# Performance work log

Hardware: AMD Instinct MI355X
Metric: run time of the kernel (lower is better)

## Reference

```python
import jax, jax.numpy as jnp
import numpy as np
from jax import lax

NUM_CLASSES = 2
IOU_THRESH = 0.5
SCORE_THRESH = 0.5
K_CAND = 512        # per-class candidate pool fed to greedy NMS
MAX_PER_CLASS = 100
MAX_TOTAL = 100


def setup_inputs() -> dict:
    key = jax.random.key(0)
    k1, k2, k3 = jax.random.split(key, 3)
    B = 64
    pred_s1 = jax.random.normal(k1, (B, 19, 19, 3, 5 + NUM_CLASSES), dtype=jnp.float32)
    pred_s2 = jax.random.normal(k2, (B, 38, 38, 3, 5 + NUM_CLASSES), dtype=jnp.float32)
    pred_s3 = jax.random.normal(k3, (B, 76, 76, 3, 5 + NUM_CLASSES), dtype=jnp.float32)
    # standard YOLOv3 anchors (pixels) normalized by input size 608
    anchors_px = np.array([[10, 13], [16, 30], [33, 23], [30, 61], [62, 45],
                           [59, 119], [116, 90], [156, 198], [373, 326]], np.float32)
    anchors = jnp.asarray(anchors_px / 608.0)
    return {"pred_s1": pred_s1, "pred_s2": pred_s2, "pred_s3": pred_s3, "anchors": anchors}


def _decode(pred, anch):
    # pred: [B, g, g, A, 5+C]; anch: [A, 2] normalized wh
    g = pred.shape[1]
    box_xy = jax.nn.sigmoid(pred[..., 0:2])
    box_wh = jnp.exp(pred[..., 2:4]) * anch          # broadcast [A,2]
    obj = jax.nn.sigmoid(pred[..., 4:5])
    cls = jax.nn.sigmoid(pred[..., 5:])
    gx, gy = jnp.meshgrid(jnp.arange(g), jnp.arange(g))   # 'xy' indexing, as tf.meshgrid
    grid = jnp.stack([gx, gy], axis=-1)[:, :, None, :].astype(pred.dtype)  # [g,g,1,2]
    xy = (box_xy + grid) / jnp.float32(g)
    x1y1 = xy - box_wh / 2.0
    x2y2 = x1y1 + box_wh                              # YoloNMS: wh + xy(top-left)
    boxes = jnp.concatenate([x1y1, x2y2], axis=-1)    # [B,g,g,A,4]
    scores = obj * cls                                # [B,g,g,A,C]
    B = pred.shape[0]
    return boxes.reshape(B, -1, 4), scores.reshape(B, -1, NUM_CLASSES)


def _pairwise_iou(b):
    # b: [K,4] in (x1,y1,x2,y2); returns [K,K]
    a = b[:, None, :]
    c = b[None, :, :]
    iw = jnp.clip(jnp.minimum(a[..., 2], c[..., 2]) - jnp.maximum(a[..., 0], c[..., 0]), 0.0)
    ih = jnp.clip(jnp.minimum(a[..., 3], c[..., 3]) - jnp.maximum(a[..., 1], c[..., 1]), 0.0)
    inter = iw * ih
    area = jnp.clip(b[:, 2] - b[:, 0], 0.0) * jnp.clip(b[:, 3] - b[:, 1], 0.0)
    union = area[:, None] + area[None, :] - inter
    return inter / jnp.maximum(union, 1e-9)


def _nms_one_class(boxes, scores):
    # boxes: [N,4], scores: [N] -> candidate boxes/scores/keep mask, each len K_CAND
    sc, idx = lax.top_k(scores, K_CAND)               # sorted descending
    bx = boxes[idx]
    iou = lax.stop_gradient(_pairwise_iou(bx))
    valid = sc > SCORE_THRESH
    def body(i, keep):
        suppressed = jnp.any(keep & (iou[i] > IOU_THRESH))
        return keep.at[i].set(valid[i] & ~suppressed)
    keep = lax.fori_loop(0, K_CAND, body, jnp.zeros((K_CAND,), jnp.bool_))
    keep = keep & (jnp.cumsum(keep) <= MAX_PER_CLASS)
    return bx, sc, keep


def _nms_one_image(boxes, scores):
    # boxes: [N,4], scores: [N,C]
    bk, sk, keep = jax.vmap(_nms_one_class, in_axes=(None, 1))(boxes, scores)  # [C,K,*]
    sm = jnp.where(keep, sk, -1.0)
    cls_ids = jnp.broadcast_to(jnp.arange(NUM_CLASSES)[:, None], (NUM_CLASSES, K_CAND))
    sf = sm.reshape(-1)
    bf = bk.reshape(-1, 4)
    cf = cls_ids.reshape(-1)
    ts, ti = lax.top_k(sf, MAX_TOTAL)
    kept = ts > 0.0
    out_boxes = jnp.where(kept[:, None], jnp.clip(bf[ti], 0.0, 1.0), 0.0)  # clip_boxes=True
    out_scores = jnp.where(kept, ts, 0.0)
    out_classes = jnp.where(kept, cf[ti].astype(jnp.float32), 0.0)
    return out_boxes, out_scores, out_classes, jnp.sum(kept).astype(jnp.int32)


def reference(pred_s1, pred_s2, pred_s3, anchors):
    # scale masks: grid19 -> anchors[6:9], grid38 -> anchors[3:6], grid76 -> anchors[0:3]
    b1, s1 = _decode(pred_s1, anchors[6:9])
    b2, s2 = _decode(pred_s2, anchors[3:6])
    b3, s3 = _decode(pred_s3, anchors[0:3])
    boxes = jnp.concatenate([b1, b2, b3], axis=1)     # [B,N,4]
    scores = jnp.concatenate([s1, s2, s3], axis=1)    # [B,N,C]
    return jax.vmap(_nms_one_image)(boxes, scores)
```

## Files before the change

### kernel.cpp

```cpp
#include <hip/hip_runtime.h>
#include <cstdint>
#include <cstddef>

#define NTOT   22743
#define N1     1083
#define N12    5415
#define BATCH  64
#define KCAND  512
#define NSEG   16
#define SEGLEN 1422
#define CAPS   384
#define CAP    4096
#define MAXPC  100
#define MAXTOT 100
#define KITER  6

__device__ __forceinline__ float sigmoidf(float x) { return 1.0f / (1.0f + expf(-x)); }
__device__ __forceinline__ int SK4(int j) { return j + ((j >> 6) << 2); }

__global__ __launch_bounds__(256) void score_filter_kernel(
    const float* __restrict__ p1, const float* __restrict__ p2,
    const float* __restrict__ p3, uint2* __restrict__ cand,
    uint32_t* __restrict__ counts)
{
  const int blk  = blockIdx.x;
  const int b    = blk >> 4;
  const int s    = blk & 15;
  const int tid  = threadIdx.x;
  const int lane = tid & 63;

  __shared__ uint2    lst[2][CAPS];
  __shared__ uint32_t lcnt[2];

  if (tid < 2) lcnt[tid] = 0u;
  __syncthreads();

  const int beg = s * SEGLEN;
  const int end = (beg + SEGLEN < NTOT) ? beg + SEGLEN : NTOT;

  float4 v[KITER];
  #pragma unroll
  for (int k = 0; k < KITER; ++k) {
    int i0 = beg + tid + k * 256;
    if (i0 < end) {
      const float* p; int local, per;
      if (i0 < N1)       { p = p1; local = i0;        per = 1083; }
      else if (i0 < N12) { p = p2; local = i0 - N1;   per = 4332; }
      else               { p = p3; local = i0 - N12;  per = 17328; }
      const float* q = p + ((size_t)b * per + local) * 7;
      v[k] = *(const float4*)(q + 3);
    } else {
      v[k] = make_float4(0.f, -1.f, 0.f, 0.f);
    }
  }

  #pragma unroll
  for (int k = 0; k < KITER; ++k) {
    int i0 = beg + tid + k * 256;
    float s0 = 0.f, s1 = 0.f;
    float q4 = v[k].y;
    if (q4 > 0.f) {
      float obj = sigmoidf(q4);
      s0 = obj * sigmoidf(v[k].z);
      s1 = obj * sigmoidf(v[k].w);
    }
    #pragma unroll
    for (int c = 0; c < 2; c++) {
      float sc = (c == 0) ? s0 : s1;
      bool pred = sc > 0.5f;
      unsigned long long m = __ballot(pred ? 1 : 0);
      if (m != 0ull) {
        int leader = (int)__ffsll(m) - 1;
        uint32_t base = 0u;
        if (lane == leader) base = atomicAdd(&lcnt[c], (uint32_t)__popcll(m));
        base = (uint32_t)__shfl((int)base, leader);
        if (pred) {
          uint32_t off = base + (uint32_t)__popcll(m & ((1ull << lane) - 1ull));
          if (off < CAPS) lst[c][off] = make_uint2(__float_as_uint(sc), (uint32_t)i0);
        }
      }
    }
  }
  __syncthreads();

  #pragma unroll
  for (int c = 0; c < 2; c++) {
    uint32_t cnt = lcnt[c]; if (cnt > CAPS) cnt = CAPS;
    uint2* dst = cand + ((size_t)((b * 2 + c) * NSEG + s)) * CAPS;
    for (uint32_t i = tid; i < cnt; i += 256) dst[i] = lst[c][i];
    if (tid == 0) counts[(b * 2 + c) * NSEG + s] = cnt;
  }
}

__device__ void decode_box(const float* __restrict__ p1, const float* __restrict__ p2,
                           const float* __restrict__ p3, const float* __restrict__ anch,
                           int b, int i, float bb[4])
{
  const float* p; int local, g, abase, per;
  if (i < N1)       { p = p1; local = i;       g = 19; abase = 6; per = 1083; }
  else if (i < N12) { p = p2; local = i - N1;  g = 38; abase = 3; per = 4332; }
  else              { p = p3; local = i - N12; g = 76; abase = 0; per = 17328; }
  const float* q = p + ((size_t)b * per + local) * 7;
  int a    = local % 3;
  int cell = local / 3;
  int col  = cell % g;
  int row  = cell / g;
  float aw = anch[(abase + a) * 2 + 0];
  float ah = anch[(abase + a) * 2 + 1];
  float x = (sigmoidf(q[0]) + (float)col) / (float)g;
  float y = (sigmoidf(q[1]) + (float)row) / (float)g;
  float w = expf(q[2]) * aw;
  float h = expf(q[3]) * ah;
  float x1 = x - w * 0.5f;
  float y1 = y - h * 0.5f;
  bb[0] = x1; bb[1] = y1; bb[2] = x1 + w; bb[3] = y1 + h;
}

__global__ __launch_bounds__(1024) void nms_kernel(
    const uint2* __restrict__ cand, const uint32_t* __restrict__ counts,
    const float* __restrict__ p1, const float* __restrict__ p2,
    const float* __restrict__ p3, const float* __restrict__ anch,
    float* __restrict__ selScore, float* __restrict__ selBox,
    int* __restrict__ selRank, int* __restrict__ selCount)
{
  const int bc   = blockIdx.x;
  const int b    = bc >> 1;
  const int tid  = threadIdx.x;
  const int lane = tid & 63;

  __shared__ __attribute__((aligned(16))) unsigned long long bord[CAP];
  __shared__ __attribute__((aligned(16))) float bx1[544];
  __shared__ __attribute__((aligned(16))) float by1[544];
  __shared__ __attribute__((aligned(16))) float bx2[544];
  __shared__ __attribute__((aligned(16))) float by2[544];
  __shared__ __attribute__((aligned(16))) float ar[544];
  __shared__ uint32_t           skey[512];
  __shared__ unsigned long long msk[128][9];
  __shared__ unsigned long long kword[8];
  __shared__ uint32_t           hist3[768];
  __shared__ uint32_t           svar[8];

  if (tid < 768) hist3[tid] = 0u;
  if (tid == 0) svar[5] = 0u;
  if (tid < 512) {
    skey[tid] = 0u; int p = SK4(tid);
    bx1[p] = 0.f; by1[p] = 0.f; bx2[p] = 0.f; by2[p] = 0.f; ar[p] = 0.f;
  }

  uint32_t pc[17];
  pc[0] = 0;
  #pragma unroll
  for (int t = 0; t < 16; ++t) {
    uint32_t c = counts[bc * NSEG + t];
    if (c > CAPS) c = CAPS;
    pc[t + 1] = pc[t] + c;
  }
  const int n = ((int)pc[16] < CAP) ? (int)pc[16] : CAP;
  const int limit = (n < KCAND) ? n : KCAND;

  unsigned long long v0, v1, v2, v3;
  auto loadc = [&](int i) -> unsigned long long {
    if (i >= n) return 0ull;
    uint32_t ps = 0; int s = 0;
    #pragma unroll
    for (int t = 1; t < 16; ++t) {
      bool ge = (uint32_t)i >= pc[t];
      s += (int)ge; ps = ge ? pc[t] : ps;
    }
    uint2 e = cand[(size_t)(bc * NSEG + s) * CAPS + (i - (int)ps)];
    return ((unsigned long long)e.x << 32) | (uint32_t)(~e.y);
  };
  v0 = loadc(tid); v1 = loadc(tid + 1024); v2 = loadc(tid + 2048); v3 = loadc(tid + 3072);
  __syncthreads();

  uint32_t* bcnt = hist3;
  uint32_t* boff = hist3 + 256;
  uint32_t* bpre = hist3 + 512;

  #define BKT(vv) ((uint32_t)(((vv) >> 47) & 255u))
  if (v0) atomicAdd(&bcnt[BKT(v0)], 1u);
  if (v1) atomicAdd(&bcnt[BKT(v1)], 1u);
  if (v2) atomicAdd(&bcnt[BKT(v2)], 1u);
  if (v3) atomicAdd(&bcnt[BKT(v3)], 1u);
  __syncthreads();

  if (tid < 64) {
    uint32_t h0 = bcnt[lane * 4 + 0], h1 = bcnt[lane * 4 + 1];
    uint32_t h2 = bcnt[lane * 4 + 2], h3 = bcnt[lane * 4 + 3];
    uint32_t s3 = h3, s2 = h2 + s3, s1 = h1 + s2, s0 = h0 + s1;
    uint32_t acc = s0;
    #pragma unroll
    for (int o = 1; o < 64; o <<= 1) {
      uint32_t vv = __shfl_down(acc, (unsigned)o);
      acc += (lane + o < 64) ? vv : 0u;
    }
    uint32_t above = acc - s0;
    bpre[lane * 4 + 0] = above + s1;
    bpre[lane * 4 + 1] = above + s2;
    bpre[lane * 4 + 2] = above + s3;
    bpre[lane * 4 + 3] = above;
  }
  __syncthreads();

  if (v0) bord[bpre[BKT(v0)] + atomicAdd(&boff[BKT(v0)], 1u)] = v0;
  if (v1) bord[bpre[BKT(v1)] + atomicAdd(&boff[BKT(v1)], 1u)] = v1;
  if (v2) bord[bpre[BKT(v2)] + atomicAdd(&boff[BKT(v2)], 1u)] = v2;
  if (v3) bord[bpre[BKT(v3)] + atomicAdd(&boff[BKT(v3)], 1u)] = v3;
  __syncthreads();

  auto rankdec = [&](unsigned long long e) {
    if (e == 0ull) return;
    const uint32_t B = BKT(e);
    const uint32_t lo = bpre[B], sz = bcnt[B];
    int rank = (int)lo;
    if ((int)lo < KCAND) {
      for (uint32_t j = lo; j < lo + sz; ++j) rank += (int)(bord[j] > e);
      if (rank < KCAND) {
        int idx = (int)(~(uint32_t)e);
        float bb[4];
        decode_box(p1, p2, p3, anch, b, idx, bb);
        int p = SK4(rank);
        bx1[p] = bb[0]; by1[p] = bb[1]; bx2[p] = bb[2]; by2[p] = bb[3];
        ar[p]  = fmaxf(bb[2] - bb[0], 0.f) * fmaxf(bb[3] - bb[1], 0.f);
        skey[rank] = (uint32_t)(e >> 32);
      }
    }
  };
  rankdec(v0); rankdec(v1); rankdec(v2); rankdec(v3);
  #undef BKT
  __syncthreads();

  unsigned long long Kw = 0ull;
  int kept = 0;
  const int r = tid & 127;
  const int w = tid >> 7;

  for (int ch = 0; ch < 4; ++ch) {
    const int base = ch * 128;
    int rows = limit - base; if (rows > 128) rows = 128;

    if (r < rows) {
      const int i = base + r;
      if (w <= (i >> 6)) {
        const int ip = SK4(i);
        const float x1i = bx1[ip], y1i = by1[ip], x2i = bx2[ip], y2i = by2[ip];
        const float ai = ar[ip];
        unsigned long long mrow = 0ull;
        #pragma unroll
        for (int m4 = 0; m4 < 16; ++m4) {
          const int j0 = (w << 6) + (m4 << 2);
          const int a  = j0 + (w << 2);
          float4 X1 = *(const float4*)&bx1[a];
          float4 Y1 = *(const float4*)&by1[a];
          float4 X2 = *(const float4*)&bx2[a];
          float4 Y2 = *(const float4*)&by2[a];
          float4 AR = *(const float4*)&ar[a];
          #define IOU_BIT(JX1,JY1,JX2,JY2,JAR,J)                              \
            { float iw = fminf(x2i,(JX2)) - fmaxf(x1i,(JX1));                 \
              float ih = fminf(y2i,(JY2)) - fmaxf(y1i,(JY1));                 \
              iw = fmaxf(iw,0.f); ih = fmaxf(ih,0.f);                        \
              float inter = iw*ih;                                            \
              float uni = fmaxf(ai + (JAR) - inter, 1e-9f);                   \
              if ((inter/uni > 0.5f) && ((J) < i))                            \
                mrow |= 1ull << ((J) & 63); }
          IOU_BIT(X1.x, Y1.x, X2.x, Y2.x, AR.x, j0 + 0)
          IOU_BIT(X1.y, Y1.y, X2.y, Y2.y, AR.y, j0 + 1)
          IOU_BIT(X1.z, Y1.z, X2.z, Y2.z, AR.z, j0 + 2)
          IOU_BIT(X1.w, Y1.w, X2.w, Y2.w, AR.w, j0 + 3)
          #undef IOU_BIT
        }
        msk[r][w] = mrow;
      } else {
        msk[r][w] = 0ull;
      }
    }
    __syncthreads();

    if (tid < 64) {
      bool stop = false;
      for (int g = 0; g < 16 && !stop; ++g) {
        int r0 = g * 8;
        if (r0 >= rows) break;
        unsigned long long wbuf[8];
        #pragma unroll
        for (int k2 = 0; k2 < 8; ++k2)
          wbuf[k2] = (lane < 8 && (r0 + k2) < rows) ? msk[r0 + k2][lane] : 0ull;
        #pragma unroll
        for (int k2 = 0; k2 < 8; ++k2) {
          if (!stop) {
            int rr = r0 + k2;
            if (rr >= rows) { stop = true; }
            else {
              int i = base + rr;
              bool ov = (Kw & wbuf[k2]) != 0ull;
              if (!__any(ov)) {
                if (lane == (i >> 6)) Kw |= 1ull << (i & 63);
                if (++kept >= MAXPC) stop = true;
              }
            }
          }
        }
      }
      if (lane == 0) svar[5] = (kept >= MAXPC || (base + (rows > 0 ? rows : 0)) >= limit) ? 1u : 0u;
    }
    __syncthreads();
    if (svar[5] != 0u) break;
  }

  if (tid < 8) kword[tid] = Kw;
  __syncthreads();

  if (tid < 512) {
    int rr = tid;
    int wr = rr >> 6;
    unsigned long long kw = kword[wr];
    if ((kw >> (rr & 63)) & 1ull) {
      uint32_t p = 0;
      for (int ww = 0; ww < wr; ++ww) p += (uint32_t)__popcll(kword[ww]);
      p += (uint32_t)__popcll(kw & ((1ull << (rr & 63)) - 1ull));
      selScore[bc * MAXPC + p] = __uint_as_float(skey[rr]);
      selRank[bc * MAXPC + p]  = rr;
      int rp = SK4(rr);
      float* o = &selBox[(size_t)(bc * MAXPC + p) * 4];
      o[0] = bx1[rp]; o[1] = by1[rp]; o[2] = bx2[rp]; o[3] = by2[rp];
    }
  }
  if (tid == 0) {
    uint32_t tot = 0;
    for (int ww = 0; ww < 8; ++ww) tot += (uint32_t)__popcll(kword[ww]);
    selCount[bc] = (int)tot;
  }
}

__global__ __launch_bounds__(256) void merge_kernel(
    const float* __restrict__ selScore, const float* __restrict__ selBox,
    const int* __restrict__ selRank, const int* __restrict__ selCount,
    float* __restrict__ out)
{
  const int b   = blockIdx.x;
  const int tid = threadIdx.x;
  __shared__ float    es[200];
  __shared__ uint32_t ek[200];
  __shared__ float    eb[200][4];
  const int c0  = selCount[b * 2 + 0];
  const int c1  = selCount[b * 2 + 1];
  const int tot = c0 + c1;

  if (tid < tot) {
    int cls  = (tid < c0) ? 0 : 1;
    int slot = (cls == 0) ? tid : (tid - c0);
    int src  = (b * 2 + cls) * MAXPC + slot;
    es[tid] = selScore[src];
    ek[tid] = (uint32_t)(cls * KCAND + selRank[src]);
    eb[tid][0] = selBox[(size_t)src * 4 + 0];
    eb[tid][1] = selBox[(size_t)src * 4 + 1];
    eb[tid][2] = selBox[(size_t)src * 4 + 2];
    eb[tid][3] = selBox[(size_t)src * 4 + 3];
  }
  __syncthreads();

  float* outBoxes  = out;
  float* outScores = out + (size_t)BATCH * MAXTOT * 4;
  float* outCls    = outScores + (size_t)BATCH * MAXTOT;
  float* outCnt    = outCls + (size_t)BATCH * MAXTOT;
  const int filled = (tot < MAXTOT) ? tot : MAXTOT;

  if (tid < tot) {
    float    s  = es[tid];
    uint32_t fk = ek[tid];
    int rank = 0;
    for (int j = 0; j < tot; j++)
      rank += (int)((es[j] > s) || (es[j] == s && ek[j] < fk));
    if (rank < MAXTOT) {
      outScores[b * MAXTOT + rank] = s;
      outCls[b * MAXTOT + rank]    = (float)(fk >> 9);
      float* ob = &outBoxes[(size_t)(b * MAXTOT + rank) * 4];
      ob[0] = fminf(fmaxf(eb[tid][0], 0.f), 1.f);
      ob[1] = fminf(fmaxf(eb[tid][1], 0.f), 1.f);
      ob[2] = fminf(fmaxf(eb[tid][2], 0.f), 1.f);
      ob[3] = fminf(fmaxf(eb[tid][3], 0.f), 1.f);
    }
  }
  if (tid >= filled && tid < MAXTOT) {
    outScores[b * MAXTOT + tid] = 0.f;
    outCls[b * MAXTOT + tid]    = 0.f;
    float* ob = &outBoxes[(size_t)(b * MAXTOT + tid) * 4];
    ob[0] = 0.f; ob[1] = 0.f; ob[2] = 0.f; ob[3] = 0.f;
  }
  if (tid == 0) outCnt[b] = (float)filled;
}

extern "C" void kernel_launch(void* const* d_in, const int* in_sizes, int n_in,
                              void* d_out, int out_size, void* d_ws, size_t ws_size,
                              hipStream_t stream)
{
  const float* p1   = (const float*)d_in[0];
  const float* p2   = (const float*)d_in[1];
  const float* p3   = (const float*)d_in[2];
  const float* anch = (const float*)d_in[3];

  uint8_t* ws = (uint8_t*)d_ws;
  uint32_t* counts = (uint32_t*)ws;
  uint2*    cand   = (uint2*)(ws + 16384);
  uint8_t*  wp     = ws + 16384 + (size_t)128 * NSEG * CAPS * 8;
  float*    selScore = (float*)wp;         wp += (size_t)BATCH * 2 * MAXPC * 4;
  float*    selBox   = (float*)wp;         wp += (size_t)BATCH * 2 * MAXPC * 16;
  int*      selRank  = (int*)wp;           wp += (size_t)BATCH * 2 * MAXPC * 4;
  int*      selCount = (int*)wp;

  score_filter_kernel<<<BATCH * NSEG, 256, 0, stream>>>(p1, p2, p3, cand, counts);
  nms_kernel<<<BATCH * 2, 1024, 0, stream>>>(cand, counts, p1, p2, p3, anch,
                                             selScore, selBox, selRank, selCount);
  merge_kernel<<<BATCH, 256, 0, stream>>>(selScore, selBox, selRank, selCount,
                                          (float*)d_out);
}
```

Before: 56.98 us.

## Fuse score filtering into per-class NMS kernel, dropping candidate workspace

Removes the separate score-filter kernel and its global candidate buffer. Each NMS block now streams its image's predictions directly, scores one class, and compacts passing candidates into shared memory with ballot-based appends, then reuses that buffer for the bucket sort. This saves a kernel launch and the global write/read round trip. In exchange, only 128 blocks scan the input (each image is read twice, once per class), so the filter phase has less parallelism. Block-to-(image,class) mapping is also permuted so the two class blocks of an image are spaced apart.

```diff
diff --git a/kernel.cpp b/kernel.cpp
--- a/kernel.cpp
+++ b/kernel.cpp
@@ -7,89 +7,26 @@
 #define N12    5415
 #define BATCH  64
 #define KCAND  512
-#define NSEG   16
-#define SEGLEN 1422
-#define CAPS   384
 #define CAP    4096
 #define MAXPC  100
 #define MAXTOT 100
-#define KITER  6
+#define KIT2   23
 
 __device__ __forceinline__ float sigmoidf(float x) { return 1.0f / (1.0f + expf(-x)); }
 __device__ __forceinline__ int SK4(int j) { return j + ((j >> 6) << 2); }
 
-__global__ __launch_bounds__(256) void score_filter_kernel(
-    const float* __restrict__ p1, const float* __restrict__ p2,
-    const float* __restrict__ p3, uint2* __restrict__ cand,
-    uint32_t* __restrict__ counts)
-{
-  const int blk  = blockIdx.x;
-  const int b    = blk >> 4;
-  const int s    = blk & 15;
-  const int tid  = threadIdx.x;
-  const int lane = tid & 63;
-
-  __shared__ uint2    lst[2][CAPS];
-  __shared__ uint32_t lcnt[2];
-
-  if (tid < 2) lcnt[tid] = 0u;
-  __syncthreads();
-
-  const int beg = s * SEGLEN;
-  const int end = (beg + SEGLEN < NTOT) ? beg + SEGLEN : NTOT;
-
-  float4 v[KITER];
-  #pragma unroll
-  for (int k = 0; k < KITER; ++k) {
-    int i0 = beg + tid + k * 256;
-    if (i0 < end) {
-      const float* p; int local, per;
-      if (i0 < N1)       { p = p1; local = i0;        per = 1083; }
-      else if (i0 < N12) { p = p2; local = i0 - N1;   per = 4332; }
-      else               { p = p3; local = i0 - N12;  per = 17328; }
-      const float* q = p + ((size_t)b * per + local) * 7;
-      v[k] = *(const float4*)(q + 3);
-    } else {
-      v[k] = make_float4(0.f, -1.f, 0.f, 0.f);
-    }
-  }
-
-  #pragma unroll
-  for (int k = 0; k < KITER; ++k) {
-    int i0 = beg + tid + k * 256;
-    float s0 = 0.f, s1 = 0.f;
-    float q4 = v[k].y;
-    if (q4 > 0.f) {
-      float obj = sigmoidf(q4);
-      s0 = obj * sigmoidf(v[k].z);
-      s1 = obj * sigmoidf(v[k].w);
-    }
-    #pragma unroll
-    for (int c = 0; c < 2; c++) {
-      float sc = (c == 0) ? s0 : s1;
-      bool pred = sc > 0.5f;
-      unsigned long long m = __ballot(pred ? 1 : 0);
-      if (m != 0ull) {
-        int leader = (int)__ffsll(m) - 1;
-        uint32_t base = 0u;
-        if (lane == leader) base = atomicAdd(&lcnt[c], (uint32_t)__popcll(m));
-        base = (uint32_t)__shfl((int)base, leader);
-        if (pred) {
-          uint32_t off = base + (uint32_t)__popcll(m & ((1ull << lane) - 1ull));
-          if (off < CAPS) lst[c][off] = make_uint2(__float_as_uint(sc), (uint32_t)i0);
-        }
-      }
-    }
-  }
-  __syncthreads();
-
-  #pragma unroll
-  for (int c = 0; c < 2; c++) {
-    uint32_t cnt = lcnt[c]; if (cnt > CAPS) cnt = CAPS;
-    uint2* dst = cand + ((size_t)((b * 2 + c) * NSEG + s)) * CAPS;
-    for (uint32_t i = tid; i < cnt; i += 256) dst[i] = lst[c][i];
-    if (tid == 0) counts[(b * 2 + c) * NSEG + s] = cnt;
-  }
+__device__ __forceinline__ float4 loadrow(const float* __restrict__ p1,
+                                          const float* __restrict__ p2,
+                                          const float* __restrict__ p3,
+                                          int b, int i)
+{
+  if (i >= NTOT) return make_float4(0.f, -1.f, 0.f, 0.f);
+  const float* p; int local, per;
+  if (i < N1)       { p = p1; local = i;        per = 1083; }
+  else if (i < N12) { p = p2; local = i - N1;   per = 4332; }
+  else              { p = p3; local = i - N12;  per = 17328; }
+  const float* q = p + ((size_t)b * per + local) * 7;
+  return *(const float4*)(q + 3);
 }
 
 __device__ void decode_box(const float* __restrict__ p1, const float* __restrict__ p2,
@@ -116,19 +53,20 @@
   bb[0] = x1; bb[1] = y1; bb[2] = x1 + w; bb[3] = y1 + h;
 }
 
-__global__ __launch_bounds__(1024) void nms_kernel(
-    const uint2* __restrict__ cand, const uint32_t* __restrict__ counts,
+__global__ __launch_bounds__(1024) void nms_fused_kernel(
     const float* __restrict__ p1, const float* __restrict__ p2,
     const float* __restrict__ p3, const float* __restrict__ anch,
     float* __restrict__ selScore, float* __restrict__ selBox,
     int* __restrict__ selRank, int* __restrict__ selCount)
 {
-  const int bc   = blockIdx.x;
-  const int b    = bc >> 1;
+  const int u    = blockIdx.x;
+  const int b    = (u & 7) | ((u >> 4) << 3);
+  const int c    = (u >> 3) & 1;
+  const int bc   = b * 2 + c;
   const int tid  = threadIdx.x;
   const int lane = tid & 63;
 
-  __shared__ __attribute__((aligned(16))) unsigned long long bord[CAP];
+  __shared__ __attribute__((aligned(16))) unsigned long long kvw[CAP];
   __shared__ __attribute__((aligned(16))) float bx1[544];
   __shared__ __attribute__((aligned(16))) float by1[544];
   __shared__ __attribute__((aligned(16))) float bx2[544];
@@ -141,36 +79,47 @@
   __shared__ uint32_t           svar[8];
 
   if (tid < 768) hist3[tid] = 0u;
-  if (tid == 0) svar[5] = 0u;
+  if (tid == 0) { svar[0] = 0u; svar[5] = 0u; }
   if (tid < 512) {
     skey[tid] = 0u; int p = SK4(tid);
     bx1[p] = 0.f; by1[p] = 0.f; bx2[p] = 0.f; by2[p] = 0.f; ar[p] = 0.f;
   }
-
-  uint32_t pc[17];
-  pc[0] = 0;
-  #pragma unroll
-  for (int t = 0; t < 16; ++t) {
-    uint32_t c = counts[bc * NSEG + t];
-    if (c > CAPS) c = CAPS;
-    pc[t + 1] = pc[t] + c;
-  }
-  const int n = ((int)pc[16] < CAP) ? (int)pc[16] : CAP;
+  __syncthreads();
+
+  float4 cur = loadrow(p1, p2, p3, b, tid);
+  for (int k = 0; k < KIT2; ++k) {
+    float4 nxt = (k + 1 < KIT2) ? loadrow(p1, p2, p3, b, (k + 1) * 1024 + tid)
+                                : make_float4(0.f, -1.f, 0.f, 0.f);
+    const int i0 = k * 1024 + tid;
+    float sc = 0.f;
+    float q4 = cur.y;
+    if (q4 > 0.f) {
+      float obj = sigmoidf(q4);
+      sc = obj * sigmoidf((c == 0) ? cur.z : cur.w);
+    }
+    bool pred = sc > 0.5f;
+    unsigned long long m = __ballot(pred ? 1 : 0);
+    if (m != 0ull) {
+      int leader = (int)__ffsll(m) - 1;
+      uint32_t base = 0u;
+      if (lane == leader) base = atomicAdd(&svar[0], (uint32_t)__popcll(m));
+      base = (uint32_t)__shfl((int)base, leader);
+      if (pred) {
+        uint32_t off = base + (uint32_t)__popcll(m & ((1ull << lane) - 1ull));
+        if (off < CAP)
+          kvw[off] = ((unsigned long long)__float_as_uint(sc) << 32) | (uint32_t)(~(uint32_t)i0);
+      }
+    }
+    cur = nxt;
+  }
+  __syncthreads();
+  const int n = ((int)svar[0] < CAP) ? (int)svar[0] : CAP;
   const int limit = (n < KCAND) ? n : KCAND;
 
-  unsigned long long v0, v1, v2, v3;
-  auto loadc = [&](int i) -> unsigned long long {
-    if (i >= n) return 0ull;
-    uint32_t ps = 0; int s = 0;
-    #pragma unroll
-    for (int t = 1; t < 16; ++t) {
-      bool ge = (uint32_t)i >= pc[t];
-      s += (int)ge; ps = ge ? pc[t] : ps;
-    }
-    uint2 e = cand[(size_t)(bc * NSEG + s) * CAPS + (i - (int)ps)];
-    return ((unsigned long long)e.x << 32) | (uint32_t)(~e.y);
-  };
-  v0 = loadc(tid); v1 = loadc(tid + 1024); v2 = loadc(tid + 2048); v3 = loadc(tid + 3072);
+  unsigned long long v0 = (tid        < n) ? kvw[tid]        : 0ull;
+  unsigned long long v1 = (tid + 1024 < n) ? kvw[tid + 1024] : 0ull;
+  unsigned long long v2 = (tid + 2048 < n) ? kvw[tid + 2048] : 0ull;
+  unsigned long long v3 = (tid + 3072 < n) ? kvw[tid + 3072] : 0ull;
   __syncthreads();
 
   uint32_t* bcnt = hist3;
@@ -202,19 +151,19 @@
   }
   __syncthreads();
 
-  if (v0) bord[bpre[BKT(v0)] + atomicAdd(&boff[BKT(v0)], 1u)] = v0;
-  if (v1) bord[bpre[BKT(v1)] + atomicAdd(&boff[BKT(v1)], 1u)] = v1;
-  if (v2) bord[bpre[BKT(v2)] + atomicAdd(&boff[BKT(v2)], 1u)] = v2;
-  if (v3) bord[bpre[BKT(v3)] + atomicAdd(&boff[BKT(v3)], 1u)] = v3;
+  if (v0) kvw[bpre[BKT(v0)] + atomicAdd(&boff[BKT(v0)], 1u)] = v0;
+  if (v1) kvw[bpre[BKT(v1)] + atomicAdd(&boff[BKT(v1)], 1u)] = v1;
+  if (v2) kvw[bpre[BKT(v2)] + atomicAdd(&boff[BKT(v2)], 1u)] = v2;
+  if (v3) kvw[bpre[BKT(v3)] + atomicAdd(&boff[BKT(v3)], 1u)] = v3;
   __syncthreads();
 
   auto rankdec = [&](unsigned long long e) {
     if (e == 0ull) return;
     const uint32_t B = BKT(e);
     const uint32_t lo = bpre[B], sz = bcnt[B];
-    int rank = (int)lo;
     if ((int)lo < KCAND) {
-      for (uint32_t j = lo; j < lo + sz; ++j) rank += (int)(bord[j] > e);
+      int rank = (int)lo;
+      for (uint32_t j = lo; j < lo + sz; ++j) rank += (int)(kvw[j] > e);
       if (rank < KCAND) {
         int idx = (int)(~(uint32_t)e);
         float bb[4];
@@ -399,18 +348,14 @@
   const float* p3   = (const float*)d_in[2];
   const float* anch = (const float*)d_in[3];
 
-  uint8_t* ws = (uint8_t*)d_ws;
-  uint32_t* counts = (uint32_t*)ws;
-  uint2*    cand   = (uint2*)(ws + 16384);
-  uint8_t*  wp     = ws + 16384 + (size_t)128 * NSEG * CAPS * 8;
-  float*    selScore = (float*)wp;         wp += (size_t)BATCH * 2 * MAXPC * 4;
-  float*    selBox   = (float*)wp;         wp += (size_t)BATCH * 2 * MAXPC * 16;
-  int*      selRank  = (int*)wp;           wp += (size_t)BATCH * 2 * MAXPC * 4;
-  int*      selCount = (int*)wp;
-
-  score_filter_kernel<<<BATCH * NSEG, 256, 0, stream>>>(p1, p2, p3, cand, counts);
-  nms_kernel<<<BATCH * 2, 1024, 0, stream>>>(cand, counts, p1, p2, p3, anch,
-                                             selScore, selBox, selRank, selCount);
+  uint8_t* wp = (uint8_t*)d_ws;
+  float*   selScore = (float*)wp;   wp += (size_t)BATCH * 2 * MAXPC * 4;
+  float*   selBox   = (float*)wp;   wp += (size_t)BATCH * 2 * MAXPC * 16;
+  int*     selRank  = (int*)wp;     wp += (size_t)BATCH * 2 * MAXPC * 4;
+  int*     selCount = (int*)wp;
+
+  nms_fused_kernel<<<BATCH * 2, 1024, 0, stream>>>(p1, p2, p3, anch,
+                                                   selScore, selBox, selRank, selCount);
   merge_kernel<<<BATCH, 256, 0, stream>>>(selScore, selBox, selRank, selCount,
                                           (float*)d_out);
 }
```

Result: slower. 61.64 us (+8.2%).
